# Performance work log

Hardware: AMD Instinct MI355X
Metric: run time of the kernel (lower is better)

The kernel has to match this reference:

```python
import jax, jax.numpy as jnp
import numpy as np

DIM = 192
HEADS = 6
WS = (2, 7, 7)
SHIFT = (1, 3, 3)
MLP_HID = int(DIM * 4.0)
N = WS[0] * WS[1] * WS[2]  # 98


def _relative_position_index():
    wt, wh, ww = WS
    coords = np.stack(np.meshgrid(np.arange(wt), np.arange(wh), np.arange(ww), indexing='ij'))
    cf = coords.reshape(3, -1)  # (3, N)
    rel = cf[:, :, None] - cf[:, None, :]  # (3, N, N)
    rel = rel.transpose(1, 2, 0).copy()
    rel[:, :, 0] += wt - 1
    rel[:, :, 1] += wh - 1
    rel[:, :, 2] += ww - 1
    rel[:, :, 0] *= (2 * wh - 1) * (2 * ww - 1)
    rel[:, :, 1] *= 2 * ww - 1
    return rel.sum(-1)  # (N, N) int

RPI = jnp.asarray(_relative_position_index())


def setup_inputs() -> dict:
    key = jax.random.key(0)
    ks = jax.random.split(key, 12)
    B, C, T, H, W = 2, DIM, 8, 56, 56
    n_bias = (2 * WS[0] - 1) * (2 * WS[1] - 1) * (2 * WS[2] - 1)
    s = lambda k, shp, sd=0.02: jax.random.normal(k, shp, jnp.float32) * sd
    return {
        'x': jax.random.normal(ks[0], (B, C, T, H, W), jnp.float32),
        'mask_matrix': jnp.zeros((256, N, N), jnp.float32),
        'norm1_g': jnp.ones((DIM,), jnp.float32),
        'norm1_b': jnp.zeros((DIM,), jnp.float32),
        'qkv_w': s(ks[1], (DIM, 3 * DIM)),
        'qkv_b': jnp.zeros((3 * DIM,), jnp.float32),
        'proj_w': s(ks[2], (DIM, DIM)),
        'proj_b': jnp.zeros((DIM,), jnp.float32),
        'rpb_table': s(ks[3], (n_bias, HEADS)),
        'norm2_g': jnp.ones((DIM,), jnp.float32),
        'norm2_b': jnp.zeros((DIM,), jnp.float32),
        'fc1_w': s(ks[4], (DIM, MLP_HID)),
        'fc1_b': jnp.zeros((MLP_HID,), jnp.float32),
        'fc2_w': s(ks[5], (MLP_HID, DIM)),
        'fc2_b': jnp.zeros((DIM,), jnp.float32),
    }


def _layernorm(x, g, b, eps=1e-5):
    mu = jnp.mean(x, -1, keepdims=True)
    var = jnp.var(x, -1, keepdims=True)
    return (x - mu) * jax.lax.rsqrt(var + eps) * g + b


def _window_partition(x):
    # x: (B, T, H, W, C) -> (B*nW, N, C)
    B, T, H, W, C = x.shape
    wt, wh, ww = WS
    x = x.reshape(B, T // wt, wt, H // wh, wh, W // ww, ww, C)
    x = x.transpose(0, 1, 3, 5, 2, 4, 6, 7)
    return x.reshape(-1, wt * wh * ww, C)


def _window_reverse(win, B, T, H, W):
    wt, wh, ww = WS
    C = win.shape[-1]
    x = win.reshape(B, T // wt, H // wh, W // ww, wt, wh, ww, C)
    x = x.transpose(0, 1, 4, 2, 5, 3, 6, 7)
    return x.reshape(B, T, H, W, C)


def reference(x, mask_matrix, norm1_g, norm1_b, qkv_w, qkv_b, proj_w, proj_b,
              rpb_table, norm2_g, norm2_b, fc1_w, fc1_b, fc2_w, fc2_b):
    B, C, T, H, W = x.shape
    hd = C // HEADS
    scale = hd ** -0.5

    shortcut = x.transpose(0, 2, 3, 4, 1)  # (B,T,H,W,C) channel-last residual
    xn = _layernorm(shortcut, norm1_g, norm1_b)
    # cyclic shift
    xs = jnp.roll(xn, shift=(-SHIFT[0], -SHIFT[1], -SHIFT[2]), axis=(1, 2, 3))
    xw = _window_partition(xs)  # (B_, N, C)
    B_ = xw.shape[0]

    qkv = (xw @ qkv_w + qkv_b).reshape(B_, N, 3, HEADS, hd)
    q, k, v = (qkv[:, :, 0].transpose(0, 2, 1, 3),
               qkv[:, :, 1].transpose(0, 2, 1, 3),
               qkv[:, :, 2].transpose(0, 2, 1, 3))  # (B_, h, N, d)
    attn = jnp.einsum('bhnd,bhmd->bhnm', q * scale, k)
    bias = rpb_table[RPI.reshape(-1)].reshape(N, N, HEADS).transpose(2, 0, 1)
    attn = attn + bias[None]
    nW = mask_matrix.shape[0]
    attn = attn.reshape(B_ // nW, nW, HEADS, N, N) + mask_matrix[None, :, None]
    attn = jax.nn.softmax(attn.reshape(B_, HEADS, N, N), axis=-1)
    out = jnp.einsum('bhnm,bhmd->bhnd', attn, v).transpose(0, 2, 1, 3).reshape(B_, N, C)
    out = out @ proj_w + proj_b

    xr = _window_reverse(out, B, T, H, W)
    xr = jnp.roll(xr, shift=SHIFT, axis=(1, 2, 3))
    x1 = shortcut + xr

    xn2 = _layernorm(x1, norm2_g, norm2_b)
    h1 = jax.nn.gelu(xn2 @ fc1_w + fc1_b, approximate=False)
    x2 = x1 + (h1 @ fc2_w + fc2_b)
    return x2.transpose(0, 4, 1, 2, 3)  # (B, C, T, H, W)
```

## Files before the change

kernel.cpp:

```cpp
#include <hip/hip_runtime.h>
#include <hip/hip_bf16.h>
#include <math.h>

#define DEV __device__ __forceinline__

typedef __bf16 bf16;
typedef __bf16 bf16x8 __attribute__((ext_vector_type(8)));
typedef float f32x4 __attribute__((ext_vector_type(4)));

DEV f32x4 zero4() { f32x4 z; z[0]=0.f; z[1]=0.f; z[2]=0.f; z[3]=0.f; return z; }

DEV void gload_lds16(const bf16* g, bf16* l) {
    __builtin_amdgcn_global_load_lds(
        (const __attribute__((address_space(1))) void*)g,
        (__attribute__((address_space(3))) void*)l, 16, 0, 0);
}

DEV float gelu_f(float v) {
    float z = 0.7978845608028654f * (v + 0.044715f * v * v * v);
    float e = __expf(-2.0f * fabsf(z));
    float t = __builtin_copysignf((1.0f - e) * __builtin_amdgcn_rcpf(1.0f + e), z);
    return 0.5f * v * (1.0f + t);
}

DEV f32x4 bmfma(bf16x8 a, bf16x8 b, f32x4 c) {
    return __builtin_amdgcn_mfma_f32_16x16x32_bf16(a, b, c, 0, 0, 0);
}


__global__ __launch_bounds__(256) void prep_w_k(
    const float* __restrict__ qw, const float* __restrict__ pw,
    const float* __restrict__ f1, const float* __restrict__ f2,
    bf16* __restrict__ qwt, bf16* __restrict__ pwt,
    bf16* __restrict__ f1t, bf16* __restrict__ f2t)
{
    int i = blockIdx.x * 256 + threadIdx.x;
    if (i < 576*192) { int n = i / 192, k = i % 192; qwt[i] = (bf16)qw[(size_t)k*576 + n]; }
    if (i < 192*192) { int n = i / 192, k = i % 192; pwt[i] = (bf16)pw[(size_t)k*192 + n]; }
    if (i < 768*192) { int n = i / 192, k = i % 192; f1t[i] = (bf16)f1[(size_t)k*768 + n]; }
    if (i < 192*768) { int n = i / 768, k = i % 768; f2t[i] = (bf16)f2[(size_t)k*192 + n]; }
}

__global__ __launch_bounds__(256) void prep_biasF_k(
    const float* __restrict__ rpb, float* __restrict__ biasF)
{
    int i = blockIdx.x * 256 + threadIdx.x;
    if (i >= 6*7*7*64) return;
    int lane = i & 63; int g = i >> 6;
    int j = g % 7; g /= 7; int rt = g % 7; int head = g / 7;
    int l15 = lane & 15, lg = lane >> 4;
    int nk = j*16 + l15;
    f32x4 o;
    #pragma unroll
    for (int r = 0; r < 4; r++) {
        int nq = rt*16 + lg*4 + r; if (nq > 97) nq = 97;
        if (nk < 98) {
            int t1 = nq/49, r1 = nq%49, h1 = r1/7, w1 = r1%7;
            int t2 = nk/49, r2 = nk%49, h2 = r2/7, w2 = r2%7;
            int idx = (t1 - t2 + 1)*169 + (h1 - h2 + 6)*13 + (w1 - w2 + 6);
            o[r] = rpb[idx*6 + head];
        } else {
            o[r] = -1e30f;
        }
    }
    *(f32x4*)&biasF[(size_t)i*4] = o;
}

__global__ __launch_bounds__(256) void prep_maskF_k(
    const float* __restrict__ maskm, float* __restrict__ maskF)
{
    int i = blockIdx.x * 256 + threadIdx.x;
    if (i >= 256*7*7*64) return;
    int lane = i & 63; int g = i >> 6;
    int j = g % 7; g /= 7; int rt = g % 7; int wib = g / 7;
    int l15 = lane & 15, lg = lane >> 4;
    int nk = j*16 + l15;
    f32x4 o;
    #pragma unroll
    for (int r = 0; r < 4; r++) {
        int nq = rt*16 + lg*4 + r; if (nq > 97) nq = 97;
        o[r] = (nk < 98) ? maskm[((size_t)wib*98 + nq)*98 + nk] : 0.f;
    }
    *(f32x4*)&maskF[(size_t)i*4] = o;
}

__global__ __launch_bounds__(256) void ln1_window_k(
    const float* __restrict__ x, const float* __restrict__ g,
    const float* __restrict__ bta, bf16* __restrict__ xw)
{
    __shared__ float tile[56*193];
    __shared__ float mu[56], rs[56];
    int blk = blockIdx.x;
    int bb = blk / 448; int r = blk % 448; int ts = r / 56; int hs = r % 56;
    int t = (ts + 1) & 7;
    int h = hs + 3; if (h >= 56) h -= 56;
    int tid = threadIdx.x;
    const float* xs = x + ((size_t)bb*1536 + t)*3136 + h*56;
    for (int e = tid; e < 192*56; e += 256) {
        int c = e / 56, w = e % 56;
        int wsp = w - 3; if (wsp < 0) wsp += 56;
        tile[wsp*193 + c] = xs[(size_t)c*25088 + w];
    }
    __syncthreads();
    if (tid < 224) {
        int row = tid >> 2, q = tid & 3;
        float s = 0.f, s2 = 0.f;
        for (int c = q*48; c < q*48 + 48; c++) {
            float v = tile[row*193 + c]; s += v; s2 += v*v;
        }
        s  += __shfl_xor(s, 1);  s  += __shfl_xor(s, 2);
        s2 += __shfl_xor(s2, 1); s2 += __shfl_xor(s2, 2);
        if (q == 0) {
            float m = s * (1.0f/192.0f);
            mu[row] = m;
            rs[row] = rsqrtf(s2 * (1.0f/192.0f) - m*m + 1e-5f);
        }
    }
    __syncthreads();
    int tb = ts >> 1, wt = ts & 1;
    int hb = hs / 7, wh = hs % 7;
    for (int e = tid; e < 56*192; e += 256) {
        int wpos = e / 192, c = e % 192;
        float v = (tile[wpos*193 + c] - mu[wpos]) * rs[wpos] * g[c] + bta[c];
        int wb = wpos / 7, ww = wpos % 7;
        int widx = bb*256 + tb*64 + hb*8 + wb;
        int n = wt*49 + wh*7 + ww;
        xw[((size_t)widx*98 + n)*192 + c] = (bf16)v;
    }
}

template<int KT, int NT, int BN, int EPI, int DB>
__global__ __launch_bounds__(256) void gemm_k(
    const bf16* __restrict__ A, const bf16* __restrict__ BT,
    const float* __restrict__ bias, const float* __restrict__ resid,
    void* __restrict__ outp)
{
    constexpr int BUFS = DB ? 2 : 1;
    __shared__ bf16 smem[BUFS*128*64 + BUFS*BN*64];
    bf16* laB = smem;
    bf16* lbB = smem + BUFS*128*64;
    constexpr int NTILES = NT / BN;
    constexpr int NK = KT / 64;
    constexpr int JT = BN / 32;
    constexpr int WN = BN / 2;
    constexpr int SPX = 392 / 8;
    int blk = blockIdx.x;
    int xcd = blk & 7, ix = blk >> 3;
    int m0 = (xcd * SPX + ix / NTILES) * 128;
    int n0 = (ix % NTILES) * BN;
    int tid = threadIdx.x;
    int lane = tid & 63;
    int wv = tid >> 6;
    int wr = wv >> 1, wc = wv & 1;
    int l15 = lane & 15, lg = lane >> 4;

    auto stage = [&](int kt, int buf) {
        int kb = kt * 64;
        #pragma unroll
        for (int t = 0; t < 4; t++) {
            int e = t*256 + wv*64 + lane;
            int row = e >> 3, ck = e & 7;
            gload_lds16(&A[(size_t)(m0 + row)*KT + kb + ((ck ^ (row & 7)) << 3)],
                        &laB[buf*128*64 + (t*256 + wv*64) * 8]);
        }
        #pragma unroll
        for (int t = 0; t < JT; t++) {
            int e = t*256 + wv*64 + lane;
            int row = e >> 3, ck = e & 7;
            gload_lds16(&BT[(size_t)(n0 + row)*KT + kb + ((ck ^ (row & 7)) << 3)],
                        &lbB[buf*BN*64 + (t*256 + wv*64) * 8]);
        }
    };

    f32x4 acc[4][JT];
    #pragma unroll
    for (int i = 0; i < 4; i++)
        #pragma unroll
        for (int j = 0; j < JT; j++) acc[i][j] = zero4();

    auto compute = [&](int cur) {
        const bf16* lab = laB + cur*128*64;
        const bf16* lbb = lbB + cur*BN*64;
        #pragma unroll
        for (int ks = 0; ks < 64; ks += 32) {
            int lc = (ks >> 3) + lg;
            bf16x8 af[4], bfr[JT];
            #pragma unroll
            for (int i = 0; i < 4; i++) {
                int ri = wr*64 + i*16 + l15;
                af[i] = *(const bf16x8*)&lab[ri*64 + ((lc ^ (ri & 7)) << 3)];
            }
            #pragma unroll
            for (int j = 0; j < JT; j++) {
                int rj = wc*WN + j*16 + l15;
                bfr[j] = *(const bf16x8*)&lbb[rj*64 + ((lc ^ (rj & 7)) << 3)];
            }
            #pragma unroll
            for (int i = 0; i < 4; i++)
                #pragma unroll
                for (int j = 0; j < JT; j++)
                    acc[i][j] = bmfma(af[i], bfr[j], acc[i][j]);
        }
    };

    if constexpr (DB) {
        stage(0, 0);
        __syncthreads();
        for (int kt = 0; kt < NK; kt++) {
            int cur = kt & 1;
            if (kt + 1 < NK) stage(kt + 1, cur ^ 1);
            compute(cur);
            __syncthreads();
        }
    } else {
        for (int kt = 0; kt < NK; kt++) {
            stage(kt, 0);
            __syncthreads();
            compute(0);
            __syncthreads();
        }
    }

    if constexpr (EPI == 4) {
        #pragma unroll
        for (int i = 0; i < 4; i++) {
            #pragma unroll
            for (int j = 0; j < JT; j++) {
                int row0 = m0 + wr*64 + i*16 + lg*4;
                int col = n0 + wc*WN + j*16 + l15;
                f32x4 o;
                #pragma unroll
                for (int r = 0; r < 4; r++)
                    o[r] = acc[i][j][r] + bias[col] + resid[(size_t)(row0 + r)*NT + col];
                int bb2 = row0 >= 25088;
                size_t off = (size_t)bb2*192*25088 + (size_t)col*25088 + (row0 - bb2*25088);
                *(f32x4*)&((float*)outp)[off] = o;
            }
        }
    } else if constexpr (EPI == 5) {
        #pragma unroll
        for (int i = 0; i < 4; i++) {
            #pragma unroll
            for (int j = 0; j < JT; j++) {
                int col = n0 + wc*WN + j*16 + l15;
                int sel = col / 192, hd = (col % 192) >> 5, d = col & 31;
                float bv = bias[col];
                #pragma unroll
                for (int r = 0; r < 4; r++) {
                    int row = m0 + wr*64 + i*16 + lg*4 + r;
                    int b_ = row / 98, n = row - b_*98;
                    size_t dst = (((size_t)b_*6 + hd)*3 + sel)*3136 + n*32 + d;
                    ((bf16*)outp)[dst] = (bf16)(acc[i][j][r] + bv);
                }
            }
        }
    } else if constexpr (EPI == 1) {
        #pragma unroll
        for (int i = 0; i < 4; i++) {
            #pragma unroll
            for (int j = 0; j < JT; j++) {
                #pragma unroll
                for (int r = 0; r < 4; r++) {
                    int row = m0 + wr*64 + i*16 + lg*4 + r;
                    int col = n0 + wc*WN + j*16 + l15;
                    ((float*)outp)[(size_t)row*NT + col] = acc[i][j][r] + bias[col];
                }
            }
        }
    } else {
        bf16* fs = smem;
        #pragma unroll
        for (int i = 0; i < 4; i++) {
            #pragma unroll
            for (int j = 0; j < JT; j++) {
                int colw = wc*WN + j*16 + l15;
                float bv = bias[n0 + colw];
                #pragma unroll
                for (int r = 0; r < 4; r++) {
                    int lr = wr*64 + i*16 + lg*4 + r;
                    fs[lr*72 + colw] = (bf16)gelu_f(acc[i][j][r] + bv);
                }
            }
        }
        __syncthreads();
        {
            int lr = tid >> 1, c0 = (tid & 1) * 32;
            size_t gbase = (size_t)(m0 + lr)*NT + n0 + c0;
            #pragma unroll
            for (int k = 0; k < 4; k++) {
                bf16x8 o = *(const bf16x8*)&fs[lr*72 + c0 + k*8];
                *(bf16x8*)&((bf16*)outp)[gbase + k*8] = o;
            }
        }
    }
}

__global__ __launch_bounds__(128) void attn_k(
    const bf16* __restrict__ qkv, const float* __restrict__ biasF,
    const float* __restrict__ maskF, bf16* __restrict__ aout)
{
    __shared__ bf16 VT[32*128];
    __shared__ bf16 Pl[2*16*136];
    int blk = blockIdx.x;
    int t8 = (blk & 7) * 384 + (blk >> 3);
    int b_ = t8 / 6, head = t8 % 6;
    int tid = threadIdx.x, lane = tid & 63, wv = tid >> 6;
    int l15 = lane & 15, lg = (lane >> 4) & 3;
    int wib = b_ & 255;
    const bf16* base = qkv + (size_t)(b_*6 + head)*3*3136;

    {
        unsigned int* vz = (unsigned int*)VT;
        for (int e = tid; e < 2048; e += 128) vz[e] = 0u;
        unsigned int* pz = (unsigned int*)Pl;
        for (int e = tid; e < 256; e += 128) {
            int w2 = e >> 7, rem = e & 127;
            int row = rem >> 3, cp = rem & 7;
            pz[(w2*16 + row)*68 + 56 + cp] = 0u;
        }
    }
    __syncthreads();
    {
        int dq = tid >> 5;
        int kl = tid & 31;
        const bf16* vbase = base + 2*3136 + dq*8;
        #pragma unroll
        for (int kr = 0; kr < 4; kr++) {
            int k = kr*32 + kl;
            if (k < 98) {
                bf16x8 v8 = *(const bf16x8*)&vbase[k*32];
                #pragma unroll
                for (int j = 0; j < 8; j++)
                    VT[(dq*8 + j)*128 + (k ^ (j << 3))] = v8[j];
            }
        }
    }
    __syncthreads();

    bf16x8 kfr[7];
    #pragma unroll
    for (int j = 0; j < 7; j++) {
        int krow = j*16 + l15; if (krow > 97) krow = 97;
        kfr[j] = *(const bf16x8*)&base[3136 + krow*32 + lg*8];
    }

    const float scale = 0.17677669529663687f;
    bf16* Pw = Pl + wv*16*136;
    const int rt0 = wv ? 4 : 0, rt1 = wv ? 7 : 4;

    auto loadQ = [&](int rt) {
        int qrow = rt*16 + l15; if (qrow > 97) qrow = 97;
        return *(const bf16x8*)&base[qrow*32 + lg*8];
    };
    bf16x8 qf = loadQ(rt0);

    #pragma unroll 1
    for (int rt = rt0; rt < rt1; rt++) {
        bf16x8 qnext = qf;
        if (rt + 1 < rt1) qnext = loadQ(rt + 1);
        f32x4 sacc[7];
        #pragma unroll
        for (int j = 0; j < 7; j++) sacc[j] = zero4();
        #pragma unroll
        for (int j = 0; j < 7; j++)
            sacc[j] = bmfma(qf, kfr[j], sacc[j]);
        {
            const float* bfp = biasF + ((size_t)(head*7 + rt)*7)*256 + lane*4;
            const float* mfp = maskF + ((size_t)(wib*7 + rt)*7)*256 + lane*4;
            #pragma unroll
            for (int j = 0; j < 7; j++) {
                f32x4 bv = *(const f32x4*)&bfp[j*256];
                f32x4 mv = *(const f32x4*)&mfp[j*256];
                sacc[j] = sacc[j]*scale + bv + mv;
            }
            f32x4 m4 = sacc[0];
            #pragma unroll
            for (int j = 1; j < 7; j++) {
                #pragma unroll
                for (int r = 0; r < 4; r++) m4[r] = fmaxf(m4[r], sacc[j][r]);
            }
            #pragma unroll
            for (int d = 1; d < 16; d <<= 1) {
                #pragma unroll
                for (int r = 0; r < 4; r++) m4[r] = fmaxf(m4[r], __shfl_xor(m4[r], d));
            }
            f32x4 s4 = zero4();
            #pragma unroll
            for (int j = 0; j < 7; j++) {
                #pragma unroll
                for (int r = 0; r < 4; r++) sacc[j][r] = __expf(sacc[j][r] - m4[r]);
                s4 += sacc[j];
            }
            #pragma unroll
            for (int d = 1; d < 16; d <<= 1) {
                #pragma unroll
                for (int r = 0; r < 4; r++) s4[r] += __shfl_xor(s4[r], d);
            }
            f32x4 inv4;
            #pragma unroll
            for (int r = 0; r < 4; r++) inv4[r] = 1.0f / s4[r];
            #pragma unroll
            for (int j = 0; j < 7; j++)
                #pragma unroll
                for (int r = 0; r < 4; r++)
                    Pw[(lg*4 + r)*136 + j*16 + l15] = (bf16)(sacc[j][r]*inv4[r]);
        }
        #pragma unroll
        for (int dt = 0; dt < 2; dt++) {
            int dl = dt*16 + l15;
            int xr = (dl & 7) << 3;
            f32x4 oacc = zero4();
            #pragma unroll
            for (int kc = 0; kc < 4; kc++) {
                bf16x8 pf = *(const bf16x8*)&Pw[l15*136 + kc*32 + lg*8];
                bf16x8 vf = *(const bf16x8*)&VT[dl*128 + ((kc*32 + lg*8) ^ xr)];
                oacc = bmfma(pf, vf, oacc);
            }
            #pragma unroll
            for (int r = 0; r < 4; r++) {
                int row = rt*16 + lg*4 + r;
                if (row < 98)
                    aout[((size_t)b_*98 + row)*192 + head*32 + dt*16 + l15] = (bf16)oacc[r];
            }
        }
        qf = qnext;
    }
}

__global__ __launch_bounds__(256) void rev_res_ln2_k(
    const float* __restrict__ x, const float* __restrict__ pw,
    const float* __restrict__ g2, const float* __restrict__ b2,
    float* __restrict__ x1, bf16* __restrict__ xn2)
{
    __shared__ float tile[56*193];
    __shared__ float mu[56], rs[56];
    int blk = blockIdx.x;
    int bb = blk / 448; int r = blk % 448; int t = r / 56; int h = r % 56;
    int ts = (t + 7) & 7;
    int hs = h - 3; if (hs < 0) hs += 56;
    int tid = threadIdx.x;
    const float* xs = x + ((size_t)bb*1536 + t)*3136 + h*56;
    for (int e = tid; e < 192*56; e += 256) {
        int c = e / 56, w = e % 56;
        tile[w*193 + c] = xs[(size_t)c*25088 + w];
    }
    __syncthreads();
    int tb = ts >> 1, wt = ts & 1, hb = hs / 7, wh = hs % 7;
    for (int e = tid; e < 56*192; e += 256) {
        int w = e / 192, c = e % 192;
        int wsp = w - 3; if (wsp < 0) wsp += 56;
        int wb = wsp / 7, ww = wsp % 7;
        size_t tok = (size_t)(bb*256 + tb*64 + hb*8 + wb)*98 + wt*49 + wh*7 + ww;
        tile[w*193 + c] += pw[tok*192 + c];
    }
    __syncthreads();
    if (tid < 224) {
        int row = tid >> 2, q = tid & 3;
        float s = 0.f, s2 = 0.f;
        for (int c = q*48; c < q*48 + 48; c++) {
            float v = tile[row*193 + c]; s += v; s2 += v*v;
        }
        s  += __shfl_xor(s, 1);  s  += __shfl_xor(s, 2);
        s2 += __shfl_xor(s2, 1); s2 += __shfl_xor(s2, 2);
        if (q == 0) {
            float m = s * (1.0f/192.0f);
            mu[row] = m;
            rs[row] = rsqrtf(s2 * (1.0f/192.0f) - m*m + 1e-5f);
        }
    }
    __syncthreads();
    size_t tok0 = ((size_t)(bb*8 + t)*56 + h)*56;
    for (int e = tid; e < 56*192; e += 256) {
        int w = e / 192, c = e % 192;
        float v = tile[w*193 + c];
        x1[(tok0 + w)*192 + c] = v;
        xn2[(tok0 + w)*192 + c] = (bf16)((v - mu[w]) * rs[w] * g2[c] + b2[c]);
    }
}

extern "C" void kernel_launch(void* const* d_in, const int* in_sizes, int n_in,
                              void* d_out, int out_size, void* d_ws, size_t ws_size,
                              hipStream_t stream)
{
    const float* x     = (const float*)d_in[0];
    const float* maskm = (const float*)d_in[1];
    const float* n1g   = (const float*)d_in[2];
    const float* n1b   = (const float*)d_in[3];
    const float* qkvw  = (const float*)d_in[4];
    const float* qkvb  = (const float*)d_in[5];
    const float* projw = (const float*)d_in[6];
    const float* projb = (const float*)d_in[7];
    const float* rpb   = (const float*)d_in[8];
    const float* n2g   = (const float*)d_in[9];
    const float* n2b   = (const float*)d_in[10];
    const float* f1w   = (const float*)d_in[11];
    const float* f1b   = (const float*)d_in[12];
    const float* f2w   = (const float*)d_in[13];
    const float* f2b   = (const float*)d_in[14];

    char* ws = (char*)d_ws;
    bf16*  qkv_wt  = (bf16*)(ws + 0);
    bf16*  proj_wt = (bf16*)(ws + 221184);
    bf16*  fc1_wt  = (bf16*)(ws + 294912);
    bf16*  fc2_wt  = (bf16*)(ws + 589824);
    float* biasF   = (float*)(ws + 884736);
    bf16* xw   = (bf16*)(ws + 1179648);
    bf16* aout = xw;
    char* Bp = ws + 1179648 + 19267584;
    bf16*  qkv  = (bf16*)Bp;
    float* pwin = (float*)Bp;
    char* Cp = Bp + 57802752;
    float* x1  = (float*)Cp;
    bf16*  xn2 = (bf16*)(Cp + 38535168);
    bf16*  h1  = (bf16*)(Cp + 38535168 + 19267584);
    float* maskF = (float*)(Cp + 38535168 + 19267584);

    prep_w_k<<<576, 256, 0, stream>>>(qkvw, projw, f1w, f2w, qkv_wt, proj_wt, fc1_wt, fc2_wt);
    prep_biasF_k<<<74, 256, 0, stream>>>(rpb, biasF);
    prep_maskF_k<<<3136, 256, 0, stream>>>(maskm, maskF);
    ln1_window_k<<<896, 256, 0, stream>>>(x, n1g, n1b, xw);
    gemm_k<192, 576, 192, 5, 0><<<392*3, 256, 0, stream>>>(xw, qkv_wt, qkvb, nullptr, qkv);
    attn_k<<<3072, 128, 0, stream>>>(qkv, biasF, maskF, aout);
    gemm_k<192, 192, 64, 1, 0><<<392*3, 256, 0, stream>>>(aout, proj_wt, projb, nullptr, pwin);
    rev_res_ln2_k<<<896, 256, 0, stream>>>(x, pwin, n2g, n2b, x1, xn2);
    gemm_k<192, 768, 64, 2, 0><<<392*12, 256, 0, stream>>>(xn2, fc1_wt, f1b, nullptr, h1);
    gemm_k<768, 192, 64, 4, 1><<<392*3, 256, 0, stream>>>(h1, fc2_wt, f2b, x1, (float*)d_out);
}
```

Before: 236.3 us.

## Fuse fc1+GELU and fc2 into a single MLP kernel keeping hidden in LDS

Replaces the two MLP GEMM launches (fc1 with GELU writing h1 to global memory, then fc2 reading it back) with one kernel. Each block loads a 64-row tile of xn2 into registers, computes 64-wide hidden chunks with GELU into LDS, and immediately accumulates them into the fc2 output. The residual add and the transposed output store happen in the same kernel. This removes the roughly 38 MB h1 round trip and one launch. In exchange, weights are read straight from global memory without LDS staging, and each block has only 4 waves with heavy register use (the A fragments stay resident).

```diff
diff --git a/kernel.cpp b/kernel.cpp
--- a/kernel.cpp
+++ b/kernel.cpp
@@ -221,23 +221,7 @@
         }
     }
 
-    if constexpr (EPI == 4) {
-        #pragma unroll
-        for (int i = 0; i < 4; i++) {
-            #pragma unroll
-            for (int j = 0; j < JT; j++) {
-                int row0 = m0 + wr*64 + i*16 + lg*4;
-                int col = n0 + wc*WN + j*16 + l15;
-                f32x4 o;
-                #pragma unroll
-                for (int r = 0; r < 4; r++)
-                    o[r] = acc[i][j][r] + bias[col] + resid[(size_t)(row0 + r)*NT + col];
-                int bb2 = row0 >= 25088;
-                size_t off = (size_t)bb2*192*25088 + (size_t)col*25088 + (row0 - bb2*25088);
-                *(f32x4*)&((float*)outp)[off] = o;
-            }
-        }
-    } else if constexpr (EPI == 5) {
+    if constexpr (EPI == 5) {
         #pragma unroll
         for (int i = 0; i < 4; i++) {
             #pragma unroll
@@ -254,7 +238,7 @@
                 }
             }
         }
-    } else if constexpr (EPI == 1) {
+    } else {
         #pragma unroll
         for (int i = 0; i < 4; i++) {
             #pragma unroll
@@ -267,30 +251,108 @@
                 }
             }
         }
-    } else {
-        bf16* fs = smem;
-        #pragma unroll
-        for (int i = 0; i < 4; i++) {
-            #pragma unroll
-            for (int j = 0; j < JT; j++) {
-                int colw = wc*WN + j*16 + l15;
-                float bv = bias[n0 + colw];
-                #pragma unroll
-                for (int r = 0; r < 4; r++) {
-                    int lr = wr*64 + i*16 + lg*4 + r;
-                    fs[lr*72 + colw] = (bf16)gelu_f(acc[i][j][r] + bv);
-                }
-            }
-        }
+    }
+}
+
+__global__ __launch_bounds__(256, 2) void mlp2_k(
+    const bf16* __restrict__ xn2, const bf16* __restrict__ f1t,
+    const bf16* __restrict__ f2t, const float* __restrict__ f1b,
+    const float* __restrict__ f2b, const float* __restrict__ x1,
+    float* __restrict__ outp)
+{
+    __shared__ bf16 xl[64*192];
+    __shared__ bf16 h1c[64*80];
+    int blk = blockIdx.x;
+    int m0 = ((blk & 7) * 98 + (blk >> 3)) * 64;
+    int tid = threadIdx.x, lane = tid & 63, wv = tid >> 6;
+    int l15 = lane & 15, lg = lane >> 4;
+
+    #pragma unroll
+    for (int t = 0; t < 6; t++) {
+        int e = t*256 + tid;
+        int row = e / 24, ko = e % 24;
+        int sw = (ko & 24) | ((ko & 7) ^ (row & 7));
+        gload_lds16(&xn2[(size_t)(m0 + row)*192 + sw*8],
+                    &xl[(t*256 + wv*64)*8]);
+    }
+    __syncthreads();
+
+    bf16x8 af[4][6];
+    #pragma unroll
+    for (int rt = 0; rt < 4; rt++) {
+        int row = rt*16 + l15;
+        #pragma unroll
+        for (int kf = 0; kf < 6; kf++) {
+            int ko = kf*4 + lg;
+            int phys = (ko & 24) | ((ko & 7) ^ (row & 7));
+            af[rt][kf] = *(const bf16x8*)&xl[row*192 + phys*8];
+        }
+    }
+
+    f32x4 acc2[4][3];
+    #pragma unroll
+    for (int a = 0; a < 4; a++)
+        #pragma unroll
+        for (int b = 0; b < 3; b++) acc2[a][b] = zero4();
+
+    for (int nc = 0; nc < 12; nc++) {
+        int hcol = nc*64 + wv*16 + l15;
+        bf16x8 b1f[6];
+        #pragma unroll
+        for (int kf = 0; kf < 6; kf++)
+            b1f[kf] = *(const bf16x8*)&f1t[(size_t)hcol*192 + kf*32 + lg*8];
+        f32x4 acc1[4];
+        #pragma unroll
+        for (int rt = 0; rt < 4; rt++) acc1[rt] = zero4();
+        #pragma unroll
+        for (int rt = 0; rt < 4; rt++)
+            #pragma unroll
+            for (int kf = 0; kf < 6; kf++)
+                acc1[rt] = bmfma(af[rt][kf], b1f[kf], acc1[rt]);
+        float bv = f1b[hcol];
+        #pragma unroll
+        for (int rt = 0; rt < 4; rt++)
+            #pragma unroll
+            for (int r = 0; r < 4; r++)
+                h1c[(rt*16 + lg*4 + r)*80 + wv*16 + l15] =
+                    (bf16)gelu_f(acc1[rt][r] + bv);
         __syncthreads();
-        {
-            int lr = tid >> 1, c0 = (tid & 1) * 32;
-            size_t gbase = (size_t)(m0 + lr)*NT + n0 + c0;
-            #pragma unroll
-            for (int k = 0; k < 4; k++) {
-                bf16x8 o = *(const bf16x8*)&fs[lr*72 + c0 + k*8];
-                *(bf16x8*)&((bf16*)outp)[gbase + k*8] = o;
-            }
+        bf16x8 b2f[3][2], a2[4][2];
+        #pragma unroll
+        for (int ct = 0; ct < 3; ct++) {
+            int col = wv*48 + ct*16 + l15;
+            #pragma unroll
+            for (int kf = 0; kf < 2; kf++)
+                b2f[ct][kf] = *(const bf16x8*)&f2t[(size_t)col*768 + nc*64 + kf*32 + lg*8];
+        }
+        #pragma unroll
+        for (int rt = 0; rt < 4; rt++)
+            #pragma unroll
+            for (int kf = 0; kf < 2; kf++)
+                a2[rt][kf] = *(const bf16x8*)&h1c[(rt*16 + l15)*80 + kf*32 + lg*8];
+        #pragma unroll
+        for (int rt = 0; rt < 4; rt++)
+            #pragma unroll
+            for (int ct = 0; ct < 3; ct++)
+                #pragma unroll
+                for (int kf = 0; kf < 2; kf++)
+                    acc2[rt][ct] = bmfma(a2[rt][kf], b2f[ct][kf], acc2[rt][ct]);
+        __syncthreads();
+    }
+
+    #pragma unroll
+    for (int rt = 0; rt < 4; rt++) {
+        #pragma unroll
+        for (int ct = 0; ct < 3; ct++) {
+            int row0 = m0 + rt*16 + lg*4;
+            int col = wv*48 + ct*16 + l15;
+            f32x4 o;
+            #pragma unroll
+            for (int r = 0; r < 4; r++)
+                o[r] = acc2[rt][ct][r] + f2b[col] + x1[(size_t)(row0 + r)*192 + col];
+            int bb2 = row0 >= 25088;
+            size_t off = (size_t)bb2*192*25088 + (size_t)col*25088 + (row0 - bb2*25088);
+            *(f32x4*)&outp[off] = o;
         }
     }
 }
@@ -512,7 +574,6 @@
     char* Cp = Bp + 57802752;
     float* x1  = (float*)Cp;
     bf16*  xn2 = (bf16*)(Cp + 38535168);
-    bf16*  h1  = (bf16*)(Cp + 38535168 + 19267584);
     float* maskF = (float*)(Cp + 38535168 + 19267584);
 
     prep_w_k<<<576, 256, 0, stream>>>(qkvw, projw, f1w, f2w, qkv_wt, proj_wt, fc1_wt, fc2_wt);
@@ -523,6 +584,5 @@
     attn_k<<<3072, 128, 0, stream>>>(qkv, biasF, maskF, aout);
     gemm_k<192, 192, 64, 1, 0><<<392*3, 256, 0, stream>>>(aout, proj_wt, projb, nullptr, pwin);
     rev_res_ln2_k<<<896, 256, 0, stream>>>(x, pwin, n2g, n2b, x1, xn2);
-    gemm_k<192, 768, 64, 2, 0><<<392*12, 256, 0, stream>>>(xn2, fc1_wt, f1b, nullptr, h1);
-    gemm_k<768, 192, 64, 4, 1><<<392*3, 256, 0, stream>>>(h1, fc2_wt, f2b, x1, (float*)d_out);
-}
+    mlp2_k<<<784, 256, 0, stream>>>(xn2, fc1_wt, fc2_wt, f1b, f2b, x1, (float*)d_out);
+}
```

After: 251.8 us. +6.5%, slower.
